# Optimization experiments

Hardware: AMD Instinct MI355X
Metric: run time of the kernel (lower is better)

The kernel has to match this reference:

```python
import jax, jax.numpy as jnp
import numpy as np

S, B, H, K = 2048, 64, 8, 12          # seq_len, input_bits, num_heads, bits per RAM neuron
N_POS = 11                             # bits for relative distance in [0, max_seq_len-1]


def setup_inputs() -> dict:
    key = jax.random.key(0)
    k1, k2, k3, k4, k5 = jax.random.split(key, 5)
    tokens = jax.random.randint(k1, (S, B), 0, 2, dtype=jnp.int32)            # bit tokens
    conn_heads = jax.random.randint(k2, (H, K), 0, 2 * B + N_POS, dtype=jnp.int32)
    head_table = jnp.round(jax.random.uniform(k3, (H, 1 << K))).astype(jnp.float32)  # {0,1} RAM cells
    conn_v = jax.random.randint(k4, (B, K), 0, B, dtype=jnp.int32)
    table_v = jnp.round(jax.random.uniform(k5, (B, 1 << K))).astype(jnp.float32)     # {0,1} RAM cells
    return {"tokens": tokens, "conn_heads": conn_heads, "head_table": head_table,
            "conn_v": conn_v, "table_v": table_v}


def reference(tokens, conn_heads, head_table, conn_v, table_v):
    pow2 = (1 << (K - 1 - jnp.arange(K))).astype(jnp.int32)                 # [K] MSB-first
    tok = tokens.astype(jnp.int32)                                           # [S,B]

    # split each head's 12 connections into query / key / relative-position groups
    grp_q = (conn_heads < B).astype(jnp.int32)
    grp_k = ((conn_heads >= B) & (conn_heads < 2 * B)).astype(jnp.int32)
    grp_p = (conn_heads >= 2 * B).astype(jnp.int32)
    cq = jnp.clip(conn_heads, 0, B - 1)
    ck = jnp.clip(conn_heads - B, 0, B - 1)
    cp = jnp.clip(conn_heads - 2 * B, 0, N_POS - 1)

    # additive address decomposition: addr(i,j,h) = addr_q(i,h)+addr_k(j,h)+addr_p(i-j,h)
    addr_q = (tok[:, cq] * (grp_q * pow2)[None]).sum(-1)                     # [S,H]
    addr_k = (tok[:, ck] * (grp_k * pow2)[None]).sum(-1)                     # [S,H]
    ar = jnp.arange(S)
    posb = ((ar[:, None] >> (N_POS - 1 - jnp.arange(N_POS))[None, :]) & 1).astype(jnp.int32)  # [S,N_POS]
    addr_p = (posb[:, cp] * (grp_p * pow2)[None]).sum(-1)                    # [S,H] indexed by rel dist

    rel = jnp.clip(ar[:, None] - ar[None, :], 0)                             # [S,S]
    addr = addr_q[:, None, :] + addr_k[None, :, :] + addr_p[rel]             # [S,S,H]

    # per-head table lookup, sum over heads = vote counts
    votes = head_table[jnp.arange(H)[None, None, :], addr].sum(-1)           # [S,S]
    causal = ar[None, :] <= ar[:, None]
    votes = jnp.where(causal, votes, 0.0)

    # bit-level value projection: one RAM neuron per output bit
    addr_v = (tok[:, conn_v] * pow2[None, None, :]).sum(-1)                  # [S,B]
    values = table_v[jnp.arange(B)[None, :], addr_v]                         # [S,B]

    # TOP_1 aggregation: first key with max vote; zeros if max vote is 0
    max_vote = votes.max(axis=1)                                             # [S]
    best = jnp.argmax(votes, axis=1)                                         # first occurrence, like the loop
    out = jnp.where((max_vote > 0)[:, None], values[best], 0.0)              # [S,B]
    return out
```

## Files before the change

### kernel.cpp

```cpp
#include <hip/hip_runtime.h>


#define SS 2048
#define BB 64
#define HH 8
#define KK 12
#define NPOS 11
#define TBL 4096
#define TBLW (TBL / 32)

typedef unsigned short u16;
typedef unsigned int u32;

__global__ __launch_bounds__(256) void precompute_kernel(
    const int* __restrict__ tokens,
    const int* __restrict__ conn_heads,
    const float* __restrict__ head_table,
    u16* __restrict__ A16, u16* __restrict__ AK16, u16* __restrict__ P16,
    u32* __restrict__ bits)
{
    int gid = blockIdx.x * blockDim.x + threadIdx.x;
    if (gid < SS * HH) {
        int s = gid >> 3;
        int h = gid & 7;
        int aq = 0, ak = 0, ap = 0;
        #pragma unroll
        for (int k = 0; k < KK; ++k) {
            int c = conn_heads[h * KK + k];
            int sh = KK - 1 - k;
            if (c < BB) {
                aq |= (tokens[s * BB + c] & 1) << sh;
            } else if (c < 2 * BB) {
                ak |= (tokens[s * BB + (c - BB)] & 1) << sh;
            } else {
                int cp = c - 2 * BB;
                ap |= ((s >> (NPOS - 1 - cp)) & 1) << sh;
            }
        }
        A16[gid]  = (u16)aq;
        AK16[gid] = (u16)ak;
        P16[gid]  = (u16)ap;
    } else {
        int w = gid - SS * HH;
        if (w < HH * TBLW) {
            int h = w >> 7;
            int wi = w & (TBLW - 1);
            u32 bv = 0;
            #pragma unroll
            for (int b = 0; b < 32; ++b) {
                if (head_table[h * TBL + wi * 32 + b] > 0.5f) bv |= (1u << b);
            }
            bits[w] = bv;
        }
    }
}

__device__ __forceinline__ int votes_packed(const u32* sbits,
                                            const uint4& q, const uint4& kk, const uint4& pp)
{
    int v = 0;
    u32 w, a0, a1;
    w = q.x | kk.x | pp.x;
    a0 = w & 0xFFFFu; a1 = w >> 16;
    v += (sbits[0 * TBLW + (a0 >> 5)] >> (a0 & 31)) & 1;
    v += (sbits[1 * TBLW + (a1 >> 5)] >> (a1 & 31)) & 1;
    w = q.y | kk.y | pp.y;
    a0 = w & 0xFFFFu; a1 = w >> 16;
    v += (sbits[2 * TBLW + (a0 >> 5)] >> (a0 & 31)) & 1;
    v += (sbits[3 * TBLW + (a1 >> 5)] >> (a1 & 31)) & 1;
    w = q.z | kk.z | pp.z;
    a0 = w & 0xFFFFu; a1 = w >> 16;
    v += (sbits[4 * TBLW + (a0 >> 5)] >> (a0 & 31)) & 1;
    v += (sbits[5 * TBLW + (a1 >> 5)] >> (a1 & 31)) & 1;
    w = q.w | kk.w | pp.w;
    a0 = w & 0xFFFFu; a1 = w >> 16;
    v += (sbits[6 * TBLW + (a0 >> 5)] >> (a0 & 31)) & 1;
    v += (sbits[7 * TBLW + (a1 >> 5)] >> (a1 & 31)) & 1;
    return v;
}

__global__ __launch_bounds__(256) void vote_kernel(
    const u16* __restrict__ A16, const u16* __restrict__ AK16, const u16* __restrict__ P16,
    const u32* __restrict__ bits_g,
    const int* __restrict__ tokens,
    const int* __restrict__ conn_v,
    const float* __restrict__ table_v,
    float* __restrict__ out)
{
    __shared__ u32 sbits[HH * TBLW];
    __shared__ u32 skey[2][4];

    const int tid = threadIdx.x;
    const int b = blockIdx.x;
    const int i0 = b;
    const int i1 = SS - 1 - b;

    ((uint4*)sbits)[tid] = ((const uint4*)bits_g)[tid];
    __syncthreads();

    const uint4 q0 = *(const uint4*)(A16 + i0 * HH);
    const uint4 q1 = *(const uint4*)(A16 + i1 * HH);

    u32 key0 = 0u, key1 = 0u;

    #pragma unroll
    for (int it = 0; it < 8; ++it) {
        const int c = (it << 8) + tid;
        const bool r0 = (c <= i0);
        const int j = r0 ? c : (c - i0 - 1);
        const int d = r0 ? (i0 - c) : (2048 - c);
        const uint4 kk = *(const uint4*)(AK16 + j * HH);
        const uint4 pp = *(const uint4*)(P16 + d * HH);
        const uint4 q = r0 ? q0 : q1;
        const int v = votes_packed(sbits, q, kk, pp);
        const u32 key = ((u32)v << 12) | (u32)(4095 - j);
        if (r0) { key0 = key0 > key ? key0 : key; }
        else    { key1 = key1 > key ? key1 : key; }
    }
    if (tid == 0) {
        const uint4 kk = *(const uint4*)(AK16 + i1 * HH);
        const uint4 pp = *(const uint4*)(P16);
        const int v = votes_packed(sbits, q1, kk, pp);
        const u32 key = ((u32)v << 12) | (u32)(4095 - i1);
        key1 = key1 > key ? key1 : key;
    }

    #pragma unroll
    for (int off = 32; off > 0; off >>= 1) {
        u32 o0 = (u32)__shfl_xor((int)key0, off, 64);
        u32 o1 = (u32)__shfl_xor((int)key1, off, 64);
        key0 = key0 > o0 ? key0 : o0;
        key1 = key1 > o1 ? key1 : o1;
    }
    if ((tid & 63) == 0) {
        skey[0][tid >> 6] = key0;
        skey[1][tid >> 6] = key1;
    }
    __syncthreads();

    if (tid < 128) {
        const int r = tid >> 6;
        const int lane = tid & 63;
        u32 ka = skey[r][0] > skey[r][1] ? skey[r][0] : skey[r][1];
        u32 kb = skey[r][2] > skey[r][3] ? skey[r][2] : skey[r][3];
        u32 kf = ka > kb ? ka : kb;
        const int row = r ? i1 : i0;
        float o = 0.0f;
        if ((kf >> 12) > 0) {
            const int best = 4095 - (int)(kf & 4095u);
            int av = 0;
            #pragma unroll
            for (int k = 0; k < KK; ++k) {
                int c = conn_v[lane * KK + k];
                av |= (tokens[best * BB + c] & 1) << (KK - 1 - k);
            }
            o = table_v[lane * TBL + av];
        }
        out[row * BB + lane] = o;
    }
}

extern "C" void kernel_launch(void* const* d_in, const int* in_sizes, int n_in,
                              void* d_out, int out_size, void* d_ws, size_t ws_size,
                              hipStream_t stream) {
    const int*   tokens     = (const int*)d_in[0];
    const int*   conn_heads = (const int*)d_in[1];
    const float* head_table = (const float*)d_in[2];
    const int*   conn_v     = (const int*)d_in[3];
    const float* table_v    = (const float*)d_in[4];
    float* out = (float*)d_out;

    int* ws = (int*)d_ws;
    u16* A16  = (u16*)ws;
    u16* AK16 = (u16*)(ws + 1 * SS * HH / 2);
    u16* P16  = (u16*)(ws + 2 * SS * HH / 2);
    u32* bits = (u32*)(ws + 3 * SS * HH / 2);

    const int total1 = SS * HH + HH * TBLW;
    precompute_kernel<<<(total1 + 255) / 256, 256, 0, stream>>>(
        tokens, conn_heads, head_table, A16, AK16, P16, bits);
    vote_kernel<<<SS / 2, 256, 0, stream>>>(
        A16, AK16, P16, bits, tokens, conn_v, table_v, out);
}
```

Baseline: 73.04 us.

## Precompute value addresses, ballot-pack table bits, batch vote loads

New measurement: 70.89 us, median of 2. 2.9% less time.

```diff
diff --git a/kernel.cpp b/kernel.cpp
--- a/kernel.cpp
+++ b/kernel.cpp
@@ -11,47 +11,60 @@
 
 typedef unsigned short u16;
 typedef unsigned int u32;
+typedef unsigned long long u64;
+
+#define SEG_A (SS * HH)
+#define SEG_B (HH * TBL)
+#define SEG_C (SS * BB)
+#define TOTAL (SEG_A + SEG_B + SEG_C)
 
 __global__ __launch_bounds__(256) void precompute_kernel(
     const int* __restrict__ tokens,
     const int* __restrict__ conn_heads,
     const float* __restrict__ head_table,
+    const int* __restrict__ conn_v,
     u16* __restrict__ A16, u16* __restrict__ AK16, u16* __restrict__ P16,
-    u32* __restrict__ bits)
+    u32* __restrict__ bits, u16* __restrict__ V16)
 {
-    int gid = blockIdx.x * blockDim.x + threadIdx.x;
-    if (gid < SS * HH) {
-        int s = gid >> 3;
-        int h = gid & 7;
+    const int gid = blockIdx.x * 256 + threadIdx.x;
+    if (gid < SEG_A) {
+        const int s = gid >> 3;
+        const int h = gid & 7;
         int aq = 0, ak = 0, ap = 0;
         #pragma unroll
         for (int k = 0; k < KK; ++k) {
-            int c = conn_heads[h * KK + k];
-            int sh = KK - 1 - k;
-            if (c < BB) {
-                aq |= (tokens[s * BB + c] & 1) << sh;
-            } else if (c < 2 * BB) {
-                ak |= (tokens[s * BB + (c - BB)] & 1) << sh;
-            } else {
-                int cp = c - 2 * BB;
-                ap |= ((s >> (NPOS - 1 - cp)) & 1) << sh;
-            }
+            const int c = conn_heads[h * KK + k];
+            const int sh = KK - 1 - k;
+            const int cq = min(c, BB - 1);
+            const int ck = min(max(c - BB, 0), BB - 1);
+            const int cp = min(max(c - 2 * BB, 0), NPOS - 1);
+            const int tq = tokens[s * BB + cq] & 1;
+            const int tk = tokens[s * BB + ck] & 1;
+            const int tp = (s >> (NPOS - 1 - cp)) & 1;
+            aq |= (c < BB ? tq : 0) << sh;
+            ap |= (c >= 2 * BB ? tp : 0) << sh;
+            ak |= ((c >= BB) && (c < 2 * BB) ? tk : 0) << sh;
         }
         A16[gid]  = (u16)aq;
         AK16[gid] = (u16)ak;
         P16[gid]  = (u16)ap;
+    } else if (gid < SEG_A + SEG_B) {
+        const int t = gid - SEG_A;
+        const u64 m = __ballot(head_table[t] > 0.5f);
+        if ((t & 63) == 0) {
+            bits[(t >> 5) + 0] = (u32)m;
+            bits[(t >> 5) + 1] = (u32)(m >> 32);
+        }
     } else {
-        int w = gid - SS * HH;
-        if (w < HH * TBLW) {
-            int h = w >> 7;
-            int wi = w & (TBLW - 1);
-            u32 bv = 0;
-            #pragma unroll
-            for (int b = 0; b < 32; ++b) {
-                if (head_table[h * TBL + wi * 32 + b] > 0.5f) bv |= (1u << b);
-            }
-            bits[w] = bv;
+        const int t = gid - (SEG_A + SEG_B);
+        const int s = t >> 6;
+        const int b = t & 63;
+        int av = 0;
+        #pragma unroll
+        for (int k = 0; k < KK; ++k) {
+            av |= (tokens[s * BB + conn_v[b * KK + k]] & 1) << (KK - 1 - k);
         }
+        V16[t] = (u16)av;
     }
 }
 
@@ -79,11 +92,10 @@
     return v;
 }
 
-__global__ __launch_bounds__(256) void vote_kernel(
+__global__ __launch_bounds__(256, 4) void vote_kernel(
     const u16* __restrict__ A16, const u16* __restrict__ AK16, const u16* __restrict__ P16,
     const u32* __restrict__ bits_g,
-    const int* __restrict__ tokens,
-    const int* __restrict__ conn_v,
+    const u16* __restrict__ V16,
     const float* __restrict__ table_v,
     float* __restrict__ out)
 {
@@ -103,16 +115,23 @@
 
     u32 key0 = 0u, key1 = 0u;
 
+    uint4 kkv[8], ppv[8];
     #pragma unroll
     for (int it = 0; it < 8; ++it) {
         const int c = (it << 8) + tid;
         const bool r0 = (c <= i0);
         const int j = r0 ? c : (c - i0 - 1);
         const int d = r0 ? (i0 - c) : (2048 - c);
-        const uint4 kk = *(const uint4*)(AK16 + j * HH);
-        const uint4 pp = *(const uint4*)(P16 + d * HH);
+        kkv[it] = *(const uint4*)(AK16 + j * HH);
+        ppv[it] = *(const uint4*)(P16 + d * HH);
+    }
+    #pragma unroll
+    for (int it = 0; it < 8; ++it) {
+        const int c = (it << 8) + tid;
+        const bool r0 = (c <= i0);
+        const int j = r0 ? c : (c - i0 - 1);
         const uint4 q = r0 ? q0 : q1;
-        const int v = votes_packed(sbits, q, kk, pp);
+        const int v = votes_packed(sbits, q, kkv[it], ppv[it]);
         const u32 key = ((u32)v << 12) | (u32)(4095 - j);
         if (r0) { key0 = key0 > key ? key0 : key; }
         else    { key1 = key1 > key ? key1 : key; }
@@ -148,13 +167,7 @@
         float o = 0.0f;
         if ((kf >> 12) > 0) {
             const int best = 4095 - (int)(kf & 4095u);
-            int av = 0;
-            #pragma unroll
-            for (int k = 0; k < KK; ++k) {
-                int c = conn_v[lane * KK + k];
-                av |= (tokens[best * BB + c] & 1) << (KK - 1 - k);
-            }
-            o = table_v[lane * TBL + av];
+            o = table_v[lane * TBL + (int)V16[best * BB + lane]];
         }
         out[row * BB + lane] = o;
     }
@@ -170,15 +183,15 @@
     const float* table_v    = (const float*)d_in[4];
     float* out = (float*)d_out;
 
-    int* ws = (int*)d_ws;
-    u16* A16  = (u16*)ws;
-    u16* AK16 = (u16*)(ws + 1 * SS * HH / 2);
-    u16* P16  = (u16*)(ws + 2 * SS * HH / 2);
-    u32* bits = (u32*)(ws + 3 * SS * HH / 2);
+    char* w = (char*)d_ws;
+    u16* A16  = (u16*)(w);
+    u16* AK16 = (u16*)(w + 32768);
+    u16* P16  = (u16*)(w + 65536);
+    u32* bits = (u32*)(w + 98304);
+    u16* V16  = (u16*)(w + 102400);
 
-    const int total1 = SS * HH + HH * TBLW;
-    precompute_kernel<<<(total1 + 255) / 256, 256, 0, stream>>>(
-        tokens, conn_heads, head_table, A16, AK16, P16, bits);
+    precompute_kernel<<<TOTAL / 256, 256, 0, stream>>>(
+        tokens, conn_heads, head_table, conn_v, A16, AK16, P16, bits, V16);
     vote_kernel<<<SS / 2, 256, 0, stream>>>(
-        A16, AK16, P16, bits, tokens, conn_v, table_v, out);
+        A16, AK16, P16, bits, V16, table_v, out);
 }
```
